# Optimization experiments

Measured on AMD Instinct MI355X. Metric: run time of the kernel, lower is better.

The kernel has to match this reference:

```python
import jax, jax.numpy as jnp
import numpy as np

# Model dims (GatedAttentionLayer of Qwen3.5 ANE hybrid stack)
C = 2048      # hidden_size
H = 16        # num_attention_heads
HK = 4        # num_key_value_heads
D = 128       # head_dim
ROT = 32      # rotary_dim = head_dim * partial_rotary_factor (0.25)
S = 1024      # sequence length (prefill)
CTX = 1024    # kv cache context length
N_ATTN = 6    # number of full-attention layers -> kv_cache leading dim 2*N_ATTN
EPS = 1e-6
ROPE_THETA = 1e7


def _rotate_half(x):
    h = x.shape[-1] // 2
    return jnp.concatenate([-x[..., h:], x[..., :h]], axis=-1)


def _rms_norm(x, w, eps=EPS):
    # Qwen3.5 convention: stored weight is (w - 1), applied as (1 + weight)
    r = jax.lax.rsqrt(jnp.mean(x * x, axis=-1, keepdims=True) + eps)
    return x * r * (1.0 + w)


def setup_inputs() -> dict:
    key = jax.random.key(0)
    ks = jax.random.split(key, 6)
    hidden_states = jax.random.normal(ks[0], (1, C, 1, S), jnp.float32)
    q_proj_w = jax.random.normal(ks[1], (H * 2 * D, C), jnp.float32) * 0.02  # q + gate
    k_proj_w = jax.random.normal(ks[2], (HK * D, C), jnp.float32) * 0.02
    v_proj_w = jax.random.normal(ks[3], (HK * D, C), jnp.float32) * 0.02
    o_proj_w = jax.random.normal(ks[4], (C, H * D), jnp.float32) * 0.02
    q_norm_w = jnp.zeros((D,), jnp.float32)
    k_norm_w = jnp.zeros((D,), jnp.float32)
    kv_cache = jnp.zeros((2 * N_ATTN, HK, CTX, D), jnp.float32)
    position_ids = jnp.arange(S, dtype=jnp.int32)
    # causal mask: 0 on/below diagonal, -1e9 above
    causal_mask = jnp.where(
        jnp.arange(CTX)[None, :] <= jnp.arange(S)[:, None], 0.0, -1e9
    ).astype(jnp.float32)[None, None]  # [1,1,S,CTX]
    # RoPE tables over rotary_dim
    inv_freq = 1.0 / (ROPE_THETA ** (jnp.arange(0, ROT, 2, dtype=jnp.float32) / ROT))
    t = jnp.arange(CTX, dtype=jnp.float32)
    freqs = jnp.outer(t, inv_freq)          # [CTX, ROT//2]
    emb = jnp.concatenate([freqs, freqs], -1)  # [CTX, ROT]
    cos_cached = jnp.cos(emb)
    sin_cached = jnp.sin(emb)
    return dict(hidden_states=hidden_states, q_proj_w=q_proj_w, k_proj_w=k_proj_w,
                v_proj_w=v_proj_w, o_proj_w=o_proj_w, q_norm_w=q_norm_w,
                k_norm_w=k_norm_w, kv_cache=kv_cache, causal_mask=causal_mask,
                position_ids=position_ids, cos_cached=cos_cached,
                sin_cached=sin_cached, attn_layer_idx=0)


def reference(hidden_states, q_proj_w, k_proj_w, v_proj_w, o_proj_w,
              q_norm_w, k_norm_w, kv_cache, causal_mask, position_ids,
              cos_cached, sin_cached, attn_layer_idx):
    x = hidden_states[0, :, 0, :]                     # [C, S]
    q_raw = q_proj_w @ x                              # [H*2D, S]  (1x1 Conv2d == GEMM)
    qg = q_raw.reshape(H, 2 * D, S)
    q = jnp.transpose(qg[:, :D, :], (0, 2, 1))        # [H, S, D]
    gate = jnp.transpose(qg[:, D:, :], (0, 2, 1))     # [H, S, D]
    k = jnp.transpose((k_proj_w @ x).reshape(HK, D, S), (0, 2, 1))  # [HK, S, D]
    v = jnp.transpose((v_proj_w @ x).reshape(HK, D, S), (0, 2, 1))  # [HK, S, D]

    q = _rms_norm(q, q_norm_w)
    k = _rms_norm(k, k_norm_w)

    cos = cos_cached[position_ids]   # [S, ROT]
    sin = sin_cached[position_ids]

    def rope(t):
        rot, pas = t[..., :ROT], t[..., ROT:]
        rot = rot * cos + _rotate_half(rot) * sin
        return jnp.concatenate([rot, pas], axis=-1)

    q, k = rope(q), rope(k)

    # prefill cache write at pos_start = position_ids[0]
    k_idx = 2 * attn_layer_idx
    v_idx = k_idx + 1
    pos_start = position_ids[0]
    kv_cache = jax.lax.dynamic_update_slice(kv_cache, k[None], (k_idx, 0, pos_start, 0))
    kv_cache = jax.lax.dynamic_update_slice(kv_cache, v[None], (v_idx, 0, pos_start, 0))

    g = H // HK  # GQA repeat (expand+reshape == contiguous repeat)
    k_full = jnp.repeat(kv_cache[k_idx], g, axis=0)   # [H, CTX, D]
    v_full = jnp.repeat(kv_cache[v_idx], g, axis=0)   # [H, CTX, D]

    scale = D ** -0.5
    attn = jnp.einsum('hsd,htd->hst', q, k_full) * scale + causal_mask[0]
    attn = jax.nn.softmax(attn, axis=-1)
    out = jnp.einsum('hst,htd->hsd', attn, v_full)    # [H, S, D]
    out = out * jax.nn.sigmoid(gate)
    out = jnp.transpose(out, (0, 2, 1)).reshape(H * D, S)
    output = (o_proj_w @ out)[None, :, None, :]       # [1, C, 1, S]
    return output
```

## Files before the change

### kernel.cpp

```cpp
#include <hip/hip_runtime.h>
#include <cstdint>

#define S_LEN 1024
#define C_DIM 2048
#define NH    16
#define NHK   4
#define HD    128
#define ROT   32
#define SCALE 0.08838834764831845f

typedef __bf16 bf16x8 __attribute__((ext_vector_type(8)));
typedef float floatx4 __attribute__((ext_vector_type(4)));
typedef float floatx16 __attribute__((ext_vector_type(16)));
typedef unsigned short ushortx8 __attribute__((ext_vector_type(8)));

__device__ __forceinline__ unsigned short f2bf(float f) {
  union { float f; uint32_t u; } x; x.f = f;
  uint32_t r = (x.u + 0x7fffu + ((x.u >> 16) & 1u)) >> 16;
  return (unsigned short)r;
}
__device__ __forceinline__ float bf2f(unsigned short v) {
  union { uint32_t u; float f; } x; x.u = (uint32_t)v << 16; return x.f;
}

__device__ __forceinline__ void async_copy16(const unsigned short* g, unsigned short* l) {
  __builtin_amdgcn_global_load_lds(
      (const __attribute__((address_space(1))) void*)g,
      (__attribute__((address_space(3))) void*)l,
      16, 0, 0);
}

__device__ __forceinline__ void bar_lds_only() {
  asm volatile("s_waitcnt lgkmcnt(0)" ::: "memory");
  __builtin_amdgcn_s_barrier();
}

__device__ __forceinline__ int swz8(int row) { return (row ^ (row >> 3)) & 7; }

__global__ __launch_bounds__(256)
void prep_kernel(const float* __restrict__ qw, const float* __restrict__ kw,
                 const float* __restrict__ vw, const float* __restrict__ ow,
                 unsigned short* __restrict__ wout,
                 const float* __restrict__ x, unsigned short* __restrict__ xT) {
  __shared__ float t[32][33];
  int bid = blockIdx.x;
  if (bid < 14336) {
    const int NQ = 4096 * 2048 / 4, NK = 512 * 2048 / 4, NV = 512 * 2048 / 4;
    int i = bid * 256 + threadIdx.x;
    const float* src; int j;
    if (i < NQ) { src = qw; j = i; }
    else if (i < NQ + NK) { src = kw; j = i - NQ; }
    else if (i < NQ + NK + NV) { src = vw; j = i - NQ - NK; }
    else { src = ow; j = i - NQ - NK - NV; }
    float4 v = ((const float4*)src)[j];
    ushort4 o;
    o.x = f2bf(v.x); o.y = f2bf(v.y); o.z = f2bf(v.z); o.w = f2bf(v.w);
    ((ushort4*)wout)[i] = o;
  } else {
    int b2 = bid - 14336;
    int st = b2 & 31, ct = b2 >> 5;
    int c = threadIdx.x & 31, rq = threadIdx.x >> 5;
#pragma unroll
    for (int i = 0; i < 4; ++i) {
      int r = rq + i * 8;
      t[r][c] = x[(size_t)(ct * 32 + r) * S_LEN + st * 32 + c];
    }
    __syncthreads();
#pragma unroll
    for (int i = 0; i < 4; ++i) {
      int r = rq + i * 8;
      xT[(size_t)(st * 32 + r) * C_DIM + ct * 32 + c] = f2bf(t[c][r]);
    }
  }
}

__device__ __forceinline__ void norm_rope_epi512(
    floatx16& acc, float (*pp)[32],
    const float* __restrict__ w, const int* __restrict__ pos_ids,
    const float* __restrict__ cosc, const float* __restrict__ sinc,
    unsigned short* __restrict__ outp,
    int wave, int lane, int wm, int scol0) {
  int l31 = lane & 31, half = lane >> 5;
  float s = 0.f;
#pragma unroll
  for (int reg = 0; reg < 16; ++reg) { float v = acc[reg]; s += v * v; }
  s += __shfl_xor(s, 32);
  if (half == 0) pp[wave][l31] = s;
  __syncthreads();
  int gb = wave & 4;
  float tot = pp[gb][l31] + pp[gb + 1][l31] + pp[gb + 2][l31] + pp[gb + 3][l31];
  float rn = rsqrtf(tot * (1.0f / 128.0f) + 1e-6f);
  int scol = scol0 + l31;
  int pos = pos_ids[scol];
  bool rope = (wm == 0);
#pragma unroll
  for (int g = 0; g < 4; ++g) {
    int dbase = wm + half * 4 + g * 8;
    ushort4 o;
#pragma unroll
    for (int rr = 0; rr < 4; ++rr) {
      int reg = g * 4 + rr;
      int d = dbase + rr;
      float v = acc[reg] * rn * (1.0f + w[d]);
      if (rope) {
        float cv = cosc[pos * ROT + d], sv = sinc[pos * ROT + d];
        int d2 = (d < 16) ? d + 16 : d - 16;
        float pv = acc[reg ^ 8] * rn * (1.0f + w[d2]);
        v = v * cv + ((d < 16) ? -pv : pv) * sv;
      }
      ((unsigned short*)&o)[rr] = f2bf(v);
    }
    *(ushort4*)&outp[(size_t)scol * HD + dbase] = o;
  }
}

#define GEMM512_CORE(EXTRA_LB)                                                     \
  int tid = threadIdx.x, wave = tid >> 6, lane = tid & 63;                         \
  int l31 = lane & 31, half = lane >> 5;                                           \
  int wm = (wave & 3) * 32, wn = (wave >> 2) * 32;                                 \
  int m0 = blockIdx.x * 128, n0 = blockIdx.y * 64;                                 \
  int r8 = tid >> 3, c8 = tid & 7;                                                 \
  int arow1 = r8 + 64;                                                             \
  int apos0 = c8 ^ swz8(r8), apos1 = c8 ^ swz8(arow1), bpos = apos0;               \
  int aswz = swz8(wm + l31), bswz = swz8(wn + l31);                                \
  const unsigned short* Ag = A + (size_t)m0 * C_DIM;                               \
  const unsigned short* Bg = BT + (size_t)n0 * C_DIM;                              \
  floatx16 acc = (floatx16)0.f;                                                    \
  ushortx8 rA0, rA1, rB;                                                           \
  rA0 = *(const ushortx8*)(Ag + (size_t)r8 * C_DIM + c8 * 8);                      \
  rA1 = *(const ushortx8*)(Ag + (size_t)arow1 * C_DIM + c8 * 8);                   \
  rB  = *(const ushortx8*)(Bg + (size_t)r8 * C_DIM + c8 * 8);                      \
  *(ushortx8*)&Asm[0][r8 * 64 + apos0 * 8] = rA0;                                  \
  *(ushortx8*)&Asm[0][arow1 * 64 + apos1 * 8] = rA1;                               \
  *(ushortx8*)&Bsm[0][r8 * 64 + bpos * 8] = rB;                                    \
  bar_lds_only();                                                                  \
  for (int t = 0; t < 32; ++t) {                                                   \
    int b = t & 1;                                                                 \
    if (t < 31) {                                                                  \
      int kt = (t + 1) * 64;                                                       \
      rA0 = *(const ushortx8*)(Ag + (size_t)r8 * C_DIM + kt + c8 * 8);             \
      rA1 = *(const ushortx8*)(Ag + (size_t)arow1 * C_DIM + kt + c8 * 8);          \
      rB  = *(const ushortx8*)(Bg + (size_t)r8 * C_DIM + kt + c8 * 8);             \
    }                                                                              \
    _Pragma("unroll")                                                              \
    for (int kb = 0; kb < 4; ++kb) {                                               \
      int ca = (((kb << 1) | half) ^ aswz) << 3;                                   \
      int cb = (((kb << 1) | half) ^ bswz) << 3;                                   \
      bf16x8 av = *(const bf16x8*)&Asm[b][(wm + l31) * 64 + ca];                   \
      bf16x8 bv = *(const bf16x8*)&Bsm[b][(wn + l31) * 64 + cb];                   \
      acc = __builtin_amdgcn_mfma_f32_32x32x16_bf16(av, bv, acc, 0, 0, 0);         \
    }                                                                              \
    if (t < 31) {                                                                  \
      *(ushortx8*)&Asm[b ^ 1][r8 * 64 + apos0 * 8] = rA0;                          \
      *(ushortx8*)&Asm[b ^ 1][arow1 * 64 + apos1 * 8] = rA1;                       \
      *(ushortx8*)&Bsm[b ^ 1][r8 * 64 + bpos * 8] = rB;                            \
    }                                                                              \
    bar_lds_only();                                                                \
  }

__global__ __launch_bounds__(512, 6)
void gemm_qkv_fused(const unsigned short* __restrict__ A,
                    const unsigned short* __restrict__ BT,
                    const float* __restrict__ qw, const float* __restrict__ kw,
                    const int* __restrict__ pos_ids,
                    const float* __restrict__ cosc, const float* __restrict__ sinc,
                    unsigned short* __restrict__ qb, unsigned short* __restrict__ kbuf,
                    unsigned short* __restrict__ vTb, unsigned short* __restrict__ sgb) {
  __shared__ unsigned short Asm[2][128 * 64];
  __shared__ unsigned short Bsm[2][64 * 64];
  __shared__ float pp[8][32];
  GEMM512_CORE()

  int scol0 = n0 + wn;
  int ty = blockIdx.x;
  if (ty < 32) {
    int h = ty >> 1;
    if ((ty & 1) == 0) {
      norm_rope_epi512(acc, pp, qw, pos_ids, cosc, sinc,
                       qb + (size_t)h * S_LEN * HD, wave, lane, wm, scol0);
    } else {
      int scol = scol0 + l31;
#pragma unroll
      for (int g = 0; g < 4; ++g) {
        int dbase = wm + half * 4 + g * 8;
        ushort4 o;
#pragma unroll
        for (int rr = 0; rr < 4; ++rr)
          ((unsigned short*)&o)[rr] = f2bf(1.0f / (1.0f + __expf(-acc[g * 4 + rr])));
        *(ushort4*)&sgb[((size_t)h * S_LEN + scol) * HD + dbase] = o;
      }
    }
  } else if (ty < 36) {
    int hk = ty - 32;
    norm_rope_epi512(acc, pp, kw, pos_ids, cosc, sinc,
                     kbuf + (size_t)hk * S_LEN * HD, wave, lane, wm, scol0);
  } else {
    int hk = ty - 36;
#pragma unroll
    for (int reg = 0; reg < 16; ++reg) {
      int d = wm + (reg & 3) + 8 * (reg >> 2) + 4 * half;
      vTb[(size_t)hk * HD * S_LEN + (size_t)d * S_LEN + scol0 + l31] = f2bf(acc[reg]);
    }
  }
}

__global__ __launch_bounds__(512, 6)
void gemm_oproj(const unsigned short* __restrict__ A,
                const unsigned short* __restrict__ BT,
                float* __restrict__ C) {
  __shared__ unsigned short Asm[2][128 * 64];
  __shared__ unsigned short Bsm[2][64 * 64];
  GEMM512_CORE()

#pragma unroll
  for (int reg = 0; reg < 16; ++reg) {
    int row = m0 + wm + (reg & 3) + 8 * (reg >> 2) + 4 * half;
    C[(size_t)row * S_LEN + n0 + wn + l31] = acc[reg];
  }
}

__global__ __launch_bounds__(256)
void attn_kernel(const unsigned short* __restrict__ qb,
                 const unsigned short* __restrict__ kbuf,
                 const unsigned short* __restrict__ vTb,
                 const unsigned short* __restrict__ sgb,
                 unsigned short* __restrict__ outT) {
  __shared__ __align__(16) unsigned short Ks[64 * 128];
  __shared__ __align__(16) unsigned short Vs[128 * 64];
  __shared__ __align__(16) unsigned short Ps[4][16][72];
  int h = blockIdx.x, qt = blockIdx.y;
  int s0 = qt * 64;
  int hk = h >> 2;
  int tid = threadIdx.x, wave = tid >> 6, lane = tid & 63;
  int l16 = lane & 15, quad = lane >> 4;
  int lsw = l16 & 7;

  const unsigned short* qg = qb + ((size_t)(h * S_LEN + s0 + wave * 16 + l16)) * HD;
  bf16x8 qfr[4];
#pragma unroll
  for (int kb = 0; kb < 4; ++kb)
    qfr[kb] = *(const bf16x8*)(qg + kb * 32 + quad * 8);

  float m_r[4], l_r[4];
#pragma unroll
  for (int r = 0; r < 4; ++r) { m_r[r] = -1e30f; l_r[r] = 0.f; }
  floatx4 acc_o[8];
#pragma unroll
  for (int i = 0; i < 8; ++i) acc_o[i] = (floatx4)0.f;
  int srow_base = s0 + wave * 16 + quad * 4;

  const unsigned short* kg0 = kbuf + (size_t)hk * S_LEN * HD;
  const unsigned short* vg0 = vTb + (size_t)hk * HD * S_LEN;

  int kr4 = lane >> 4, kc16 = lane & 15;
  int vr8 = lane >> 3, vc8 = lane & 7;

  for (int t = 0; t <= qt; ++t) {
    int jt = t * 64;
#pragma unroll
    for (int i = 0; i < 4; ++i) {
      int rbase = wave * 16 + i * 4;
      int row = rbase + kr4;
      int cs = kc16 ^ (row & 7);
      async_copy16(kg0 + (size_t)(jt + row) * HD + cs * 8, Ks + rbase * 128);
    }
#pragma unroll
    for (int i = 0; i < 4; ++i) {
      int rbase = wave * 32 + i * 8;
      int row = rbase + vr8;
      int cs = vc8 ^ (row & 7);
      async_copy16(vg0 + (size_t)row * S_LEN + jt + cs * 8, Vs + rbase * 64);
    }
    __syncthreads();

    floatx4 acc_s[4];
#pragma unroll
    for (int ni = 0; ni < 4; ++ni) acc_s[ni] = (floatx4)0.f;
#pragma unroll
    for (int kb = 0; kb < 4; ++kb) {
#pragma unroll
      for (int ni = 0; ni < 4; ++ni) {
        int cl = (kb * 4 + quad) ^ lsw;
        bf16x8 bk = *(const bf16x8*)&Ks[(ni * 16 + l16) * 128 + cl * 8];
        acc_s[ni] = __builtin_amdgcn_mfma_f32_16x16x32_bf16(qfr[kb], bk, acc_s[ni], 0, 0, 0);
      }
    }

    bool diag = (t == qt);
    float alpha[4];
#pragma unroll
    for (int r = 0; r < 4; ++r) {
      float scv[4];
      float mx = -1e30f;
#pragma unroll
      for (int ni = 0; ni < 4; ++ni) {
        float sv = acc_s[ni][r] * SCALE;
        if (diag) {
          int jg = jt + ni * 16 + l16;
          if (jg > srow_base + r) sv = -1e30f;
        }
        scv[ni] = sv;
        mx = fmaxf(mx, sv);
      }
#pragma unroll
      for (int off = 8; off; off >>= 1) mx = fmaxf(mx, __shfl_xor(mx, off, 16));
      float mnew = fmaxf(m_r[r], mx);
      float psv = 0.f;
#pragma unroll
      for (int ni = 0; ni < 4; ++ni) {
        float pv = (scv[ni] > -1e29f) ? __expf(scv[ni] - mnew) : 0.f;
        Ps[wave][quad * 4 + r][ni * 16 + l16] = f2bf(pv);
        psv += pv;
      }
#pragma unroll
      for (int off = 8; off; off >>= 1) psv += __shfl_xor(psv, off, 16);
      alpha[r] = __expf(m_r[r] - mnew);
      m_r[r] = mnew;
      l_r[r] = l_r[r] * alpha[r] + psv;
    }
#pragma unroll
    for (int i = 0; i < 8; ++i)
#pragma unroll
      for (int r = 0; r < 4; ++r) acc_o[i][r] *= alpha[r];
    __threadfence_block();

#pragma unroll
    for (int kb2 = 0; kb2 < 2; ++kb2) {
      bf16x8 ap = *(const bf16x8*)&Ps[wave][l16][kb2 * 32 + quad * 8];
#pragma unroll
      for (int ni2 = 0; ni2 < 8; ++ni2) {
        int cl = (kb2 * 4 + quad) ^ lsw;
        bf16x8 bv = *(const bf16x8*)&Vs[(ni2 * 16 + l16) * 64 + cl * 8];
        acc_o[ni2] = __builtin_amdgcn_mfma_f32_16x16x32_bf16(ap, bv, acc_o[ni2], 0, 0, 0);
      }
    }
    __syncthreads();
  }

#pragma unroll
  for (int r = 0; r < 4; ++r) {
    int s = srow_base + r;
    float inv = 1.0f / l_r[r];
    const unsigned short* sgp = sgb + ((size_t)h * S_LEN + s) * HD;
    unsigned short* op = outT + (size_t)s * (NH * HD) + h * HD;
#pragma unroll
    for (int ni2 = 0; ni2 < 8; ++ni2) {
      int d = ni2 * 16 + l16;
      op[d] = f2bf(acc_o[ni2][r] * inv * bf2f(sgp[d]));
    }
  }
}

extern "C" void kernel_launch(void* const* d_in, const int* in_sizes, int n_in,
                              void* d_out, int out_size, void* d_ws, size_t ws_size,
                              hipStream_t stream) {
  const float* hs       = (const float*)d_in[0];
  const float* q_proj_w = (const float*)d_in[1];
  const float* k_proj_w = (const float*)d_in[2];
  const float* v_proj_w = (const float*)d_in[3];
  const float* o_proj_w = (const float*)d_in[4];
  const float* q_norm_w = (const float*)d_in[5];
  const float* k_norm_w = (const float*)d_in[6];
  const int*   pos_ids  = (const int*)d_in[9];
  const float* cos_c    = (const float*)d_in[10];
  const float* sin_c    = (const float*)d_in[11];
  float* out = (float*)d_out;

  char* ws = (char*)d_ws;
  unsigned short* wqkv = (unsigned short*)(ws + 0);
  unsigned short* wo   = (unsigned short*)(ws + 20971520);
  unsigned short* xT   = (unsigned short*)(ws + 29360128);
  unsigned short* qb   = (unsigned short*)(ws + 33554432);
  unsigned short* kbuf = (unsigned short*)(ws + 37748736);
  unsigned short* vTb  = (unsigned short*)(ws + 38797312);
  unsigned short* sgb  = (unsigned short*)(ws + 39845888);
  unsigned short* aoT  = (unsigned short*)(ws + 44040192);

  prep_kernel<<<14336 + 2048, 256, 0, stream>>>(q_proj_w, k_proj_w, v_proj_w, o_proj_w,
                                                wqkv, hs, xT);
  gemm_qkv_fused<<<dim3(40, 16), 512, 0, stream>>>(wqkv, xT, q_norm_w, k_norm_w,
                                                   pos_ids, cos_c, sin_c,
                                                   qb, kbuf, vTb, sgb);
  attn_kernel<<<dim3(16, 16), 256, 0, stream>>>(qb, kbuf, vTb, sgb, aoT);
  gemm_oproj<<<dim3(16, 16), 512, 0, stream>>>(wo, aoT, out);
}
```

Measured before the change: 241.6 us.

## Split attention KV range into two chunks with separate merge kernel

Applies a flash-decoding style split to the causal attention. The KV tile loop is divided into chunks of 8 tiles along a new grid z dimension, and each block writes unnormalized partial outputs plus row max and row sum to fp32 workspace. A new merge kernel combines the two partials with log-sum-exp weights, then applies the sigmoid gate and writes the bf16 output. The aim is to balance the uneven causal work across more blocks and raise parallelism from 256 blocks. The cost is an extra launch and fp32 partial traffic through global memory.

```diff
diff --git a/kernel.cpp b/kernel.cpp
--- a/kernel.cpp
+++ b/kernel.cpp
@@ -223,12 +223,15 @@
 void attn_kernel(const unsigned short* __restrict__ qb,
                  const unsigned short* __restrict__ kbuf,
                  const unsigned short* __restrict__ vTb,
-                 const unsigned short* __restrict__ sgb,
-                 unsigned short* __restrict__ outT) {
+                 float* __restrict__ pm, float* __restrict__ pl,
+                 float* __restrict__ pO) {
   __shared__ __align__(16) unsigned short Ks[64 * 128];
   __shared__ __align__(16) unsigned short Vs[128 * 64];
   __shared__ __align__(16) unsigned short Ps[4][16][72];
-  int h = blockIdx.x, qt = blockIdx.y;
+  int h = blockIdx.x, qt = blockIdx.y, ch = blockIdx.z;
+  int t0 = ch * 8;
+  if (t0 > qt) return;
+  int t1 = min(qt, t0 + 7);
   int s0 = qt * 64;
   int hk = h >> 2;
   int tid = threadIdx.x, wave = tid >> 6, lane = tid & 63;
@@ -255,7 +258,7 @@
   int kr4 = lane >> 4, kc16 = lane & 15;
   int vr8 = lane >> 3, vc8 = lane & 7;
 
-  for (int t = 0; t <= qt; ++t) {
+  for (int t = t0; t <= t1; ++t) {
     int jt = t * 64;
 #pragma unroll
     for (int i = 0; i < 4; ++i) {
@@ -337,17 +340,56 @@
     __syncthreads();
   }
 
+  size_t pbase = ((size_t)(h * 16 + qt) * 2 + ch);
+  float* pOp = pO + pbase * 8192;
 #pragma unroll
   for (int r = 0; r < 4; ++r) {
-    int s = srow_base + r;
-    float inv = 1.0f / l_r[r];
-    const unsigned short* sgp = sgb + ((size_t)h * S_LEN + s) * HD;
-    unsigned short* op = outT + (size_t)s * (NH * HD) + h * HD;
-#pragma unroll
-    for (int ni2 = 0; ni2 < 8; ++ni2) {
-      int d = ni2 * 16 + l16;
-      op[d] = f2bf(acc_o[ni2][r] * inv * bf2f(sgp[d]));
-    }
+    int rrow = wave * 16 + quad * 4 + r;
+    if (l16 == 0) { pm[pbase * 64 + rrow] = m_r[r]; pl[pbase * 64 + rrow] = l_r[r]; }
+#pragma unroll
+    for (int ni2 = 0; ni2 < 8; ++ni2)
+      pOp[rrow * 128 + ni2 * 16 + l16] = acc_o[ni2][r];
+  }
+}
+
+__global__ __launch_bounds__(256)
+void attn_merge(const float* __restrict__ pm, const float* __restrict__ pl,
+                const float* __restrict__ pO,
+                const unsigned short* __restrict__ sgb,
+                unsigned short* __restrict__ outT) {
+  int h = blockIdx.x, qt = blockIdx.y;
+  int vc = (qt >= 8) ? 2 : 1;
+  size_t b0 = ((size_t)(h * 16 + qt) * 2);
+  const float* O0 = pO + b0 * 8192;
+  const float* O1 = O0 + 8192;
+  int lane32 = threadIdx.x & 31, rb = threadIdx.x >> 5;
+  int d = lane32 * 4;
+#pragma unroll
+  for (int rr = 0; rr < 8; ++rr) {
+    int row = rr * 8 + rb;
+    float m0 = pm[b0 * 64 + row], l0 = pl[b0 * 64 + row];
+    float w0 = 1.f, w1 = 0.f;
+    float L = l0;
+    if (vc == 2) {
+      float m1 = pm[(b0 + 1) * 64 + row], l1 = pl[(b0 + 1) * 64 + row];
+      float M = fmaxf(m0, m1);
+      w0 = __expf(m0 - M); w1 = __expf(m1 - M);
+      L = w0 * l0 + w1 * l1;
+    }
+    float inv = 1.0f / L;
+    floatx4 o = *(const floatx4*)&O0[row * 128 + d];
+    if (vc == 2) {
+      floatx4 o1 = *(const floatx4*)&O1[row * 128 + d];
+#pragma unroll
+      for (int j = 0; j < 4; ++j) o[j] = o[j] * w0 + o1[j] * w1;
+    }
+    int s = qt * 64 + row;
+    ushort4 sg4 = *(const ushort4*)&sgb[((size_t)h * S_LEN + s) * HD + d];
+    ushort4 out4;
+#pragma unroll
+    for (int j = 0; j < 4; ++j)
+      ((unsigned short*)&out4)[j] = f2bf(o[j] * inv * bf2f(((unsigned short*)&sg4)[j]));
+    *(ushort4*)&outT[(size_t)s * (NH * HD) + h * HD + d] = out4;
   }
 }
 
@@ -375,12 +417,16 @@
   unsigned short* vTb  = (unsigned short*)(ws + 38797312);
   unsigned short* sgb  = (unsigned short*)(ws + 39845888);
   unsigned short* aoT  = (unsigned short*)(ws + 44040192);
+  float*          pO   = (float*)(ws + 48234496);
+  float*          pm   = (float*)(ws + 65011712);
+  float*          pl   = (float*)(ws + 65142784);
 
   prep_kernel<<<14336 + 2048, 256, 0, stream>>>(q_proj_w, k_proj_w, v_proj_w, o_proj_w,
                                                 wqkv, hs, xT);
   gemm_qkv_fused<<<dim3(40, 16), 512, 0, stream>>>(wqkv, xT, q_norm_w, k_norm_w,
                                                    pos_ids, cos_c, sin_c,
                                                    qb, kbuf, vTb, sgb);
-  attn_kernel<<<dim3(16, 16), 256, 0, stream>>>(qb, kbuf, vTb, sgb, aoT);
+  attn_kernel<<<dim3(16, 16, 2), 256, 0, stream>>>(qb, kbuf, vTb, pm, pl, pO);
+  attn_merge<<<dim3(16, 16), 256, 0, stream>>>(pm, pl, pO, sgb, aoT);
   gemm_oproj<<<dim3(16, 16), 512, 0, stream>>>(wo, aoT, out);
 }
```

Result: no change. 238.8 us (-1.2%).

## Double-buffer K tiles and prefetch next K/V in attention loop

Applied to the files above, without the earlier changes.

The attention kernel now double-buffers the K tile in LDS. It issues the async global-to-LDS load for the next K tile before computing QK^T on the current one, and loads the next V tile right after the PV MMAs. Full __syncthreads calls are replaced by explicit vmcnt waits plus raw s_barrier, so memory latency overlaps with the MFMA and softmax work. In exchange it uses more LDS per block, which may reduce occupancy, and it depends on vmcnt counting for correctness.

```diff
diff --git a/kernel.cpp b/kernel.cpp
--- a/kernel.cpp
+++ b/kernel.cpp
@@ -29,6 +29,8 @@
       (__attribute__((address_space(3))) void*)l,
       16, 0, 0);
 }
+
+#define WAIT_VM(N) asm volatile("s_waitcnt vmcnt(" #N ")" ::: "memory")
 
 __device__ __forceinline__ void bar_lds_only() {
   asm volatile("s_waitcnt lgkmcnt(0)" ::: "memory");
@@ -225,7 +227,7 @@
                  const unsigned short* __restrict__ vTb,
                  const unsigned short* __restrict__ sgb,
                  unsigned short* __restrict__ outT) {
-  __shared__ __align__(16) unsigned short Ks[64 * 128];
+  __shared__ __align__(16) unsigned short Ks[2][64 * 128];
   __shared__ __align__(16) unsigned short Vs[128 * 64];
   __shared__ __align__(16) unsigned short Ps[4][16][72];
   int h = blockIdx.x, qt = blockIdx.y;
@@ -240,6 +242,8 @@
 #pragma unroll
   for (int kb = 0; kb < 4; ++kb)
     qfr[kb] = *(const bf16x8*)(qg + kb * 32 + quad * 8);
+  asm volatile("" :: "v"(qfr[0]), "v"(qfr[1]), "v"(qfr[2]), "v"(qfr[3]));
+  WAIT_VM(0);
 
   float m_r[4], l_r[4];
 #pragma unroll
@@ -255,23 +259,32 @@
   int kr4 = lane >> 4, kc16 = lane & 15;
   int vr8 = lane >> 3, vc8 = lane & 7;
 
+#define STAGE_K(BUF, T)                                                    \
+  { _Pragma("unroll")                                                      \
+    for (int i = 0; i < 4; ++i) {                                          \
+      int rbase = wave * 16 + i * 4;                                       \
+      int row = rbase + kr4;                                               \
+      int cs = kc16 ^ (row & 7);                                           \
+      async_copy16(kg0 + (size_t)((T) * 64 + row) * HD + cs * 8,           \
+                   &Ks[BUF][rbase * 128]); } }
+#define STAGE_V(T)                                                         \
+  { _Pragma("unroll")                                                      \
+    for (int i = 0; i < 4; ++i) {                                          \
+      int rbase = wave * 32 + i * 8;                                       \
+      int row = rbase + vr8;                                               \
+      int cs = vc8 ^ (row & 7);                                            \
+      async_copy16(vg0 + (size_t)row * S_LEN + (T) * 64 + cs * 8,          \
+                   Vs + rbase * 64); } }
+
+  STAGE_K(0, 0)
+  STAGE_V(0)
+
   for (int t = 0; t <= qt; ++t) {
-    int jt = t * 64;
-#pragma unroll
-    for (int i = 0; i < 4; ++i) {
-      int rbase = wave * 16 + i * 4;
-      int row = rbase + kr4;
-      int cs = kc16 ^ (row & 7);
-      async_copy16(kg0 + (size_t)(jt + row) * HD + cs * 8, Ks + rbase * 128);
-    }
-#pragma unroll
-    for (int i = 0; i < 4; ++i) {
-      int rbase = wave * 32 + i * 8;
-      int row = rbase + vr8;
-      int cs = vc8 ^ (row & 7);
-      async_copy16(vg0 + (size_t)row * S_LEN + jt + cs * 8, Vs + rbase * 64);
-    }
-    __syncthreads();
+    int cur = t & 1;
+    bool more = (t < qt);
+    if (more) { STAGE_K(cur ^ 1, t + 1) WAIT_VM(8); }
+    else      { WAIT_VM(4); }
+    __builtin_amdgcn_s_barrier();
 
     floatx4 acc_s[4];
 #pragma unroll
@@ -281,11 +294,12 @@
 #pragma unroll
       for (int ni = 0; ni < 4; ++ni) {
         int cl = (kb * 4 + quad) ^ lsw;
-        bf16x8 bk = *(const bf16x8*)&Ks[(ni * 16 + l16) * 128 + cl * 8];
+        bf16x8 bk = *(const bf16x8*)&Ks[cur][(ni * 16 + l16) * 128 + cl * 8];
         acc_s[ni] = __builtin_amdgcn_mfma_f32_16x16x32_bf16(qfr[kb], bk, acc_s[ni], 0, 0, 0);
       }
     }
 
+    int jt = t * 64;
     bool diag = (t == qt);
     float alpha[4];
 #pragma unroll
@@ -322,7 +336,10 @@
     for (int i = 0; i < 8; ++i)
 #pragma unroll
       for (int r = 0; r < 4; ++r) acc_o[i][r] *= alpha[r];
-    __threadfence_block();
+
+    if (more) { WAIT_VM(4); }
+    else      { WAIT_VM(0); }
+    __builtin_amdgcn_s_barrier();
 
 #pragma unroll
     for (int kb2 = 0; kb2 < 2; ++kb2) {
@@ -334,7 +351,8 @@
         acc_o[ni2] = __builtin_amdgcn_mfma_f32_16x16x32_bf16(ap, bv, acc_o[ni2], 0, 0, 0);
       }
     }
-    __syncthreads();
+    __builtin_amdgcn_s_barrier();
+    if (more) { STAGE_V(t + 1) }
   }
 
 #pragma unroll
@@ -349,6 +367,8 @@
       op[d] = f2bf(acc_o[ni2][r] * inv * bf2f(sgp[d]));
     }
   }
+#undef STAGE_K
+#undef STAGE_V
 }
 
 extern "C" void kernel_launch(void* const* d_in, const int* in_sizes, int n_in,
```

Measured after the change: 240.6 us. Within noise of the previous version (-0.4%).
